# Performance work log

Measured on AMD Instinct MI355X. Metric: run time of the kernel, lower is better.

The kernel has to match this reference:

```python
import jax, jax.numpy as jnp
import numpy as np

D = 768      # embedding_dim
M = 3072     # mlp_dim
G = 4        # num_expert_groups
E = 8        # experts_per_group
KG = 2       # k_groups
KE = 4       # k_experts
EPS = 1e-6   # gate weight threshold from the torch module


def setup_inputs() -> dict:
    key = jax.random.key(0)
    ks = jax.random.split(key, 9)
    x = jax.random.normal(ks[0], (1, 1024, D), dtype=jnp.float32)
    Wg = jax.random.normal(ks[1], (D, G), dtype=jnp.float32) * 0.02
    bg = jax.random.normal(ks[2], (G,), dtype=jnp.float32) * 0.01
    We = jax.random.normal(ks[3], (G, D, E), dtype=jnp.float32) * 0.02
    be = jax.random.normal(ks[4], (G, E), dtype=jnp.float32) * 0.01
    W1 = jax.random.normal(ks[5], (G, E, D, M), dtype=jnp.float32) * 0.02
    b1 = jax.random.normal(ks[6], (G, E, M), dtype=jnp.float32) * 0.01
    W2 = jax.random.normal(ks[7], (G, E, M, D), dtype=jnp.float32) * 0.02
    b2 = jax.random.normal(ks[8], (G, E, D), dtype=jnp.float32) * 0.01
    return {"x": x, "Wg": Wg, "bg": bg, "We": We, "be": be,
            "W1": W1, "b1": b1, "W2": W2, "b2": b2}


def _topk_gates(logits, k):
    # top-k logits -> softmax over the k entries, then zero out weights < 1e-6
    top, idx = jax.lax.top_k(logits, k)
    gates = jax.nn.softmax(top, axis=-1)
    gates = jnp.where(gates >= EPS, gates, jnp.zeros_like(gates))
    return gates, idx


def reference(x, Wg, bg, We, be, W1, b1, W2, b2):
    orig_shape = x.shape
    xf = x.reshape(-1, D)  # [N, D]

    # ---- level 1: group gating (eval mode: clean logits, no noise) ----
    glog = xf @ Wg + bg                      # [N, G]
    ggates, gidx = _topk_gates(glog, KG)     # [N, KG]
    gw = jnp.einsum('nk,nkg->ng', ggates,
                    jax.nn.one_hot(gidx, G, dtype=xf.dtype))  # dense [N, G]

    # ---- level 2: expert gating within each group ----
    # computed densely for all groups; unselected groups get zero group weight
    elog = jnp.einsum('nd,gde->nge', xf, We) + be  # [N, G, E]
    egates, eidx = _topk_gates(elog, KE)            # [N, G, KE]
    ew = jnp.einsum('ngk,ngke->nge', egates,
                    jax.nn.one_hot(eidx, E, dtype=xf.dtype))  # dense [N, G, E]

    combine = gw[:, :, None] * ew  # [N, G, E] combine weights

    # ---- expert MLPs (dense compute, combine-weighted sum) ----
    y = jnp.zeros_like(xf)
    for g in range(G):  # small fixed loop over expert groups
        h = jax.nn.gelu(jnp.einsum('nd,edm->enm', xf, W1[g]) + b1[g][:, None, :],
                        approximate=False)               # [E, N, M]
        o = jnp.einsum('enm,emd->end', h, W2[g]) + b2[g][:, None, :]  # [E, N, D]
        y = y + jnp.einsum('end,ne->nd', o, combine[:, g, :])
    return y.reshape(orig_shape)
```

## Files before the change

### kernel.cpp

```cpp
#include <hip/hip_runtime.h>
#include <hip/hip_bf16.h>
#include <math.h>

#define NTOK 1024
#define DDIM 768
#define MDIM 3072
#define GN 4
#define EN 8
#define NEXP 32
#define NPAIR 8192
#define EPSW 1e-6f
#define MAXRB 96

typedef __attribute__((ext_vector_type(4))) float f32x4;
typedef __attribute__((ext_vector_type(4))) int   i32x4;
typedef __attribute__((ext_vector_type(4))) unsigned short u16x4;
typedef __attribute__((ext_vector_type(8))) __bf16 bf16x8;

__device__ __forceinline__ unsigned short f2bf(float f) {
  unsigned u = __builtin_bit_cast(unsigned, f);
  u += 0x7FFFu + ((u >> 16) & 1u);
  return (unsigned short)(u >> 16);
}

__device__ __forceinline__ unsigned cvt_pk_bf16(float lo, float hi) {
  unsigned r;
  asm volatile("v_cvt_pk_bf16_f32 %0, %1, %2" : "=v"(r) : "v"(lo), "v"(hi));
  return r;
}

__device__ __forceinline__ void gld_lds16(const void* g, void* l) {
  __builtin_amdgcn_global_load_lds(
      (const __attribute__((address_space(1))) void*)g,
      (__attribute__((address_space(3))) void*)l, 16, 0, 0);
}

__global__ void init_kernel(int* __restrict__ p) { p[threadIdx.x] = 0; }

__global__ __launch_bounds__(256) void zero_y(float* __restrict__ y) {
  ((f32x4*)y)[blockIdx.x * 256 + threadIdx.x] = (f32x4){0.f, 0.f, 0.f, 0.f};
}

__global__ __launch_bounds__(256) void x2bf(const float* __restrict__ x,
                                            unsigned short* __restrict__ xb) {
  const int i = (blockIdx.x * 256 + threadIdx.x) * 16;
#pragma unroll
  for (int j = 0; j < 4; ++j) {
    const f32x4 v = *(const f32x4*)(x + i + j * 4);
    u16x4 p = { f2bf(v.x), f2bf(v.y), f2bf(v.z), f2bf(v.w) };
    *(u16x4*)(xb + i + j * 4) = p;
  }
}

__global__ __launch_bounds__(256) void gating_kernel(
    const float* __restrict__ x, const float* __restrict__ Wg,
    const float* __restrict__ bg, const float* __restrict__ We,
    const float* __restrict__ be, int* __restrict__ counts,
    int* __restrict__ pair_e, float* __restrict__ pair_w)
{
  __shared__ float xr[DDIM];
  __shared__ float logits[36];
  const int n = blockIdx.x;
  const int tid = threadIdx.x;
  const float* xp = x + (size_t)n * DDIM;
  for (int d = tid; d < DDIM; d += 256) xr[d] = xp[d];
  __syncthreads();

  const int w = tid >> 6, lane = tid & 63;
  for (int j = 0; j < 9; ++j) {
    const int o = w + 4 * j;
    float s = 0.f;
    if (o < 4) {
      for (int d = lane; d < DDIM; d += 64) s += xr[d] * Wg[d * GN + o];
    } else {
      const int g = (o - 4) >> 3, e = (o - 4) & 7;
      const float* wp = We + (size_t)g * DDIM * EN + e;
      for (int d = lane; d < DDIM; d += 64) s += xr[d] * wp[d * EN];
    }
    for (int off = 32; off; off >>= 1) s += __shfl_xor(s, off);
    if (lane == 0) logits[o] = s + ((o < 4) ? bg[o] : be[o - 4]);
  }
  __syncthreads();

  if (tid == 0) {
    float gl[4];
    for (int i = 0; i < 4; ++i) gl[i] = logits[i];
    int i0 = 0;
    for (int i = 1; i < 4; ++i) if (gl[i] > gl[i0]) i0 = i;
    int i1 = -1;
    for (int i = 0; i < 4; ++i) {
      if (i == i0) continue;
      if (i1 < 0 || gl[i] > gl[i1]) i1 = i;
    }
    const float m = gl[i0];
    const float e1 = expf(gl[i1] - m);
    const float s2 = 1.f + e1;
    float gv[2] = { 1.f / s2, e1 / s2 };
    int gi[2] = { i0, i1 };
    for (int r = 0; r < 2; ++r) if (gv[r] < EPSW) gv[r] = 0.f;

    for (int r = 0; r < 2; ++r) {
      const int g = gi[r];
      float el[8];
      for (int e = 0; e < 8; ++e) el[e] = logits[4 + g * 8 + e];
      int sel[4];
      for (int q = 0; q < 4; ++q) {
        int best = -1;
        for (int e = 0; e < 8; ++e) {
          bool used = false;
          for (int p = 0; p < q; ++p) if (sel[p] == e) used = true;
          if (used) continue;
          if (best < 0 || el[e] > el[best]) best = e;
        }
        sel[q] = best;
      }
      const float mm = el[sel[0]];
      float ex[4]; float ss = 0.f;
      for (int q = 0; q < 4; ++q) { ex[q] = expf(el[sel[q]] - mm); ss += ex[q]; }
      for (int q = 0; q < 4; ++q) {
        float ew = ex[q] / ss;
        if (ew < EPSW) ew = 0.f;
        const int gbl = g * 8 + sel[q];
        const int j = r * 4 + q;
        pair_e[n * 8 + j] = gbl;
        pair_w[n * 8 + j] = gv[r] * ew;
        atomicAdd(&counts[gbl], 1);
      }
    }
  }
}

__global__ void scan_kernel(const int* __restrict__ counts, int* __restrict__ offsets,
                            int* __restrict__ rb_ge, int* __restrict__ rb_by,
                            int* __restrict__ nrb)
{
  if (threadIdx.x == 0) {
    int a = 0, n = 0;
    for (int e = 0; e < NEXP; ++e) {
      offsets[e] = a;
      const int c = counts[e];
      a += c;
      for (int b = 0; b * 128 < c; ++b) { rb_ge[n] = e; rb_by[n] = b; ++n; }
    }
    *nrb = n;
  }
}

__global__ __launch_bounds__(256) void scatter_kernel(
    const int* __restrict__ pair_e, const float* __restrict__ pair_w,
    const int* __restrict__ offsets, int* __restrict__ cursor,
    int* __restrict__ slot_tok, float* __restrict__ slot_w)
{
  const int idx = blockIdx.x * 256 + threadIdx.x;
  if (idx < NPAIR) {
    const int e = pair_e[idx];
    const int s = offsets[e] + atomicAdd(&cursor[e], 1);
    slot_tok[s] = idx >> 3;
    slot_w[s] = pair_w[idx];
  }
}

template<int K, int NLD, int EPI, int GATHER, int KS>
__global__ __launch_bounds__(256, 2) void moe_gemm_gl(
    const unsigned short* __restrict__ Abase, const float* __restrict__ W,
    const float* __restrict__ bias, const int* __restrict__ counts,
    const int* __restrict__ offsets, const float* __restrict__ slot_w,
    const int* __restrict__ slot_tok, const int* __restrict__ rb_ge,
    const int* __restrict__ rb_by, const int* __restrict__ nrb,
    unsigned short* __restrict__ Hout, float* __restrict__ Yout)
{
  constexpr int KC = K / KS;
  constexpr int NT = KC / 32;
  constexpr int ABY = 8192;
  constexpr int FBY = 16384;
  constexpr int BBY = 8192;
  constexpr int BUFB = ABY + FBY + BBY;

  const int rb = blockIdx.x;
  if (rb >= *nrb) return;
  const int ge = rb_ge[rb];
  const int by = rb_by[rb];
  const int cnt = counts[ge];
  const int off = offsets[ge];
  const int nb = blockIdx.y;
  const int ks = (KS > 1) ? blockIdx.z : 0;
  const int kbase = ks * KC;
  const int tid = threadIdx.x;

  __shared__ __align__(16) unsigned char lds[2 * BUFB];

  const unsigned short* asrc[2];
#pragma unroll
  for (int i = 0; i < 2; ++i) {
    const int q = tid + 256 * i;
    const int m = q >> 2, c = q & 3;
    const int sc = c ^ ((m ^ (m >> 2)) & 3);
    int gr = by * 128 + m; if (gr >= cnt) gr = cnt - 1;
    const int row = GATHER ? slot_tok[off + gr] : (off + gr);
    asrc[i] = Abase + (size_t)row * K + kbase + sc * 8;
  }

  const float* fsrc[4];
#pragma unroll
  for (int i = 0; i < 4; ++i) {
    const int q = tid + 256 * i;
    fsrc[i] = W + (size_t)ge * K * NLD + (size_t)(kbase + (q >> 5)) * NLD
                + nb * 128 + (q & 31) * 4;
  }

  const int tn = tid & 127;
  const int tk0 = (tid >> 7) * 16;
  const int tsn = (tn ^ (tn >> 2)) & 3;

  const int w = tid >> 6, lane = tid & 63;
  const int wr = (w >> 1) * 64, wc = (w & 1) * 64;
  const int l15 = lane & 15, l4 = lane >> 4;
  int aoff[4], boff[4];
#pragma unroll
  for (int mf = 0; mf < 4; ++mf) {
    const int m = wr + mf * 16 + l15;
    aoff[mf] = m * 64 + ((l4 ^ ((m ^ (m >> 2)) & 3)) * 16);
  }
#pragma unroll
  for (int nf = 0; nf < 4; ++nf) {
    const int n = wc + nf * 16 + l15;
    boff[nf] = ABY + FBY + n * 64 + ((l4 ^ ((n ^ (n >> 2)) & 3)) * 16);
  }

  f32x4 acc[4][4];
#pragma unroll
  for (int mf = 0; mf < 4; ++mf)
#pragma unroll
    for (int nf = 0; nf < 4; ++nf)
      acc[mf][nf] = (f32x4){0.f, 0.f, 0.f, 0.f};

#define ISSUE(T, BASE) { \
    _Pragma("unroll") \
    for (int i = 0; i < 2; ++i) \
      gld_lds16(asrc[i] + (size_t)(T) * 32, (BASE) + (tid + 256 * i) * 16); \
    _Pragma("unroll") \
    for (int i = 0; i < 4; ++i) \
      gld_lds16(fsrc[i] + (size_t)(T) * 32 * NLD, (BASE) + ABY + (tid + 256 * i) * 16); }
#define TRANS(BASE) { \
    const float* fp = (const float*)((BASE) + ABY); \
    unsigned char* bb = (BASE) + ABY + FBY; \
    float fv[16]; \
    _Pragma("unroll") \
    for (int j = 0; j < 16; ++j) fv[j] = fp[(tk0 + j) * 128 + tn]; \
    _Pragma("unroll") \
    for (int jp = 0; jp < 8; ++jp) { \
      const unsigned wv = cvt_pk_bf16(fv[2 * jp], fv[2 * jp + 1]); \
      const int c = (tk0 * 2 + 4 * jp) >> 4; \
      *(unsigned*)(bb + tn * 64 + ((c ^ tsn) * 16) + ((4 * jp) & 15)) = wv; } }
#define COMPUTE(BASE) { bf16x8 afr[4], bfr[4]; _Pragma("unroll") \
    for (int mf = 0; mf < 4; ++mf) \
      afr[mf] = __builtin_bit_cast(bf16x8, *(const i32x4*)((BASE) + aoff[mf])); \
    _Pragma("unroll") \
    for (int nf = 0; nf < 4; ++nf) \
      bfr[nf] = __builtin_bit_cast(bf16x8, *(const i32x4*)((BASE) + boff[nf])); \
    _Pragma("unroll") \
    for (int mf = 0; mf < 4; ++mf) { _Pragma("unroll") \
      for (int nf = 0; nf < 4; ++nf) \
        acc[mf][nf] = __builtin_amdgcn_mfma_f32_16x16x32_bf16( \
            afr[mf], bfr[nf], acc[mf][nf], 0, 0, 0); } }

  ISSUE(0, lds);

  for (int t = 0; t < NT; ++t) {
    unsigned char* buf = lds + (t & 1) * BUFB;
    unsigned char* obuf = lds + ((t + 1) & 1) * BUFB;
    asm volatile("s_waitcnt vmcnt(0)" ::: "memory");
    __builtin_amdgcn_s_barrier();
    asm volatile("" ::: "memory");
    if (t + 1 < NT) ISSUE(t + 1, obuf);
    TRANS(buf);
    asm volatile("s_waitcnt lgkmcnt(0)" ::: "memory");
    __builtin_amdgcn_s_barrier();
    asm volatile("" ::: "memory");
    COMPUTE(buf);
  }
#undef ISSUE
#undef TRANS
#undef COMPUTE

#pragma unroll
  for (int mf = 0; mf < 4; ++mf) {
    const int rb2 = by * 128 + wr + mf * 16 + l4 * 4;
    if constexpr (EPI == 0) {
#pragma unroll
      for (int nf = 0; nf < 4; ++nf) {
        const int col = nb * 128 + wc + nf * 16 + l15;
        const float bv = bias[(size_t)ge * NLD + col];
#pragma unroll
        for (int j = 0; j < 4; ++j) {
          const int r = rb2 + j;
          if (r < cnt) {
            const float v = acc[mf][nf][j] + bv;
            const float gl = 0.5f * v * (1.f + erff(v * 0.70710678118654752f));
            Hout[(size_t)(off + r) * NLD + col] = f2bf(gl);
          }
        }
      }
    } else {
#pragma unroll
      for (int j = 0; j < 4; ++j) {
        const int r = rb2 + j;
        if (r < cnt) {
          const int slot = off + r;
          const float sw = slot_w[slot];
          const int tok = slot_tok[slot];
#pragma unroll
          for (int nf = 0; nf < 4; ++nf) {
            const int col = nb * 128 + wc + nf * 16 + l15;
            const float bv = (ks == 0) ? bias[(size_t)ge * NLD + col] : 0.f;
            atomicAdd(&Yout[(size_t)tok * DDIM + col], sw * (acc[mf][nf][j] + bv));
          }
        }
      }
    }
  }
}

extern "C" void kernel_launch(void* const* d_in, const int* in_sizes, int n_in,
                              void* d_out, int out_size, void* d_ws, size_t ws_size,
                              hipStream_t stream)
{
  const float* x  = (const float*)d_in[0];
  const float* Wg = (const float*)d_in[1];
  const float* bg = (const float*)d_in[2];
  const float* We = (const float*)d_in[3];
  const float* be = (const float*)d_in[4];
  const float* W1 = (const float*)d_in[5];
  const float* b1 = (const float*)d_in[6];
  const float* W2 = (const float*)d_in[7];
  const float* b2 = (const float*)d_in[8];
  float* y = (float*)d_out;

  char* ws = (char*)d_ws;
  int*   counts   = (int*)(ws + 0);
  int*   offsets  = (int*)(ws + 128);
  int*   cursor   = (int*)(ws + 256);
  int*   nrb      = (int*)(ws + 384);
  int*   rb_ge    = (int*)(ws + 512);
  int*   rb_by    = (int*)(ws + 896);
  int*   pair_e   = (int*)(ws + 2048);
  float* pair_w   = (float*)(ws + 34816);
  int*   slot_tok = (int*)(ws + 67584);
  float* slot_w   = (float*)(ws + 100352);
  unsigned short* xb = (unsigned short*)(ws + 135168);
  unsigned short* H  = (unsigned short*)(ws + 12715008);

  init_kernel<<<1, 256, 0, stream>>>((int*)ws);
  zero_y<<<NTOK * DDIM / 1024, 256, 0, stream>>>(y);
  x2bf<<<NTOK * DDIM / 4096, 256, 0, stream>>>(x, xb);
  gating_kernel<<<NTOK, 256, 0, stream>>>(x, Wg, bg, We, be, counts, pair_e, pair_w);
  scan_kernel<<<1, 64, 0, stream>>>(counts, offsets, rb_ge, rb_by, nrb);
  scatter_kernel<<<NPAIR / 256, 256, 0, stream>>>(pair_e, pair_w, offsets, cursor,
                                                  slot_tok, slot_w);

  moe_gemm_gl<DDIM, MDIM, 0, 1, 1><<<dim3(MAXRB, MDIM / 128, 1), 256, 0, stream>>>(
      xb, W1, b1, counts, offsets, nullptr, slot_tok, rb_ge, rb_by, nrb, H, nullptr);
  moe_gemm_gl<MDIM, DDIM, 1, 0, 2><<<dim3(MAXRB, DDIM / 128, 2), 256, 0, stream>>>(
      H, W2, b2, counts, offsets, slot_w, slot_tok, rb_ge, rb_by, nrb, nullptr, y);
}
```

Baseline: 562.1 us.

## Pre-repack expert weights to transposed bf16 and deepen GEMM prefetch pipeline

Adds a repack kernel that transposes each expert's fp32 W1/W2 into a K-contiguous bf16 buffer before each GEMM. The grouped GEMM then loads bf16 B tiles straight into LDS, with no per-tile fp32-to-bf16 transpose in LDS. The main loop now keeps two tiles in flight (prefetch distance 2) with a partial vmcnt wait. The cost is a full pass over all 32 experts' weights every call, including experts that get no tokens, plus extra workspace.

```diff
diff --git a/kernel.cpp b/kernel.cpp
--- a/kernel.cpp
+++ b/kernel.cpp
@@ -23,16 +23,15 @@
   return (unsigned short)(u >> 16);
 }
 
-__device__ __forceinline__ unsigned cvt_pk_bf16(float lo, float hi) {
-  unsigned r;
-  asm volatile("v_cvt_pk_bf16_f32 %0, %1, %2" : "=v"(r) : "v"(lo), "v"(hi));
-  return r;
-}
-
 __device__ __forceinline__ void gld_lds16(const void* g, void* l) {
   __builtin_amdgcn_global_load_lds(
       (const __attribute__((address_space(1))) void*)g,
       (__attribute__((address_space(3))) void*)l, 16, 0, 0);
+}
+
+template<int N>
+__device__ __forceinline__ void wait_vmcnt() {
+  asm volatile("s_waitcnt vmcnt(%0)" :: "n"(N) : "memory");
 }
 
 __global__ void init_kernel(int* __restrict__ p) { p[threadIdx.x] = 0; }
@@ -160,9 +159,36 @@
   }
 }
 
+template<int R, int C>
+__global__ __launch_bounds__(256) void repack_kernel(
+    const float* __restrict__ W, unsigned short* __restrict__ Wt)
+{
+  __shared__ float tile[32][33];
+  const int ge = blockIdx.z;
+  const int rt = blockIdx.y, ct = blockIdx.x;
+  const int tid = threadIdx.x;
+  {
+    const int r = tid >> 3, c4 = tid & 7;
+    const f32x4 v = *(const f32x4*)(W + (size_t)ge * R * C
+                                      + (size_t)(rt * 32 + r) * C + ct * 32 + c4 * 4);
+#pragma unroll
+    for (int j = 0; j < 4; ++j) tile[r][c4 * 4 + j] = v[j];
+  }
+  __syncthreads();
+  {
+    const int n = tid >> 3, k4 = tid & 7;
+    u16x4 p;
+    p.x = f2bf(tile[k4 * 4 + 0][n]);
+    p.y = f2bf(tile[k4 * 4 + 1][n]);
+    p.z = f2bf(tile[k4 * 4 + 2][n]);
+    p.w = f2bf(tile[k4 * 4 + 3][n]);
+    *(u16x4*)(Wt + (size_t)ge * R * C + (size_t)(ct * 32 + n) * R + rt * 32 + k4 * 4) = p;
+  }
+}
+
 template<int K, int NLD, int EPI, int GATHER, int KS>
-__global__ __launch_bounds__(256, 2) void moe_gemm_gl(
-    const unsigned short* __restrict__ Abase, const float* __restrict__ W,
+__global__ __launch_bounds__(256) void moe_gemm_bt2(
+    const unsigned short* __restrict__ A, const unsigned short* __restrict__ Bt,
     const float* __restrict__ bias, const int* __restrict__ counts,
     const int* __restrict__ offsets, const float* __restrict__ slot_w,
     const int* __restrict__ slot_tok, const int* __restrict__ rb_ge,
@@ -172,9 +198,7 @@
   constexpr int KC = K / KS;
   constexpr int NT = KC / 32;
   constexpr int ABY = 8192;
-  constexpr int FBY = 16384;
-  constexpr int BBY = 8192;
-  constexpr int BUFB = ABY + FBY + BBY;
+  constexpr int BUFB = 16384;
 
   const int rb = blockIdx.x;
   if (rb >= *nrb) return;
@@ -190,6 +214,7 @@
   __shared__ __align__(16) unsigned char lds[2 * BUFB];
 
   const unsigned short* asrc[2];
+  const unsigned short* bsrc[2];
 #pragma unroll
   for (int i = 0; i < 2; ++i) {
     const int q = tid + 256 * i;
@@ -197,20 +222,9 @@
     const int sc = c ^ ((m ^ (m >> 2)) & 3);
     int gr = by * 128 + m; if (gr >= cnt) gr = cnt - 1;
     const int row = GATHER ? slot_tok[off + gr] : (off + gr);
-    asrc[i] = Abase + (size_t)row * K + kbase + sc * 8;
-  }
-
-  const float* fsrc[4];
-#pragma unroll
-  for (int i = 0; i < 4; ++i) {
-    const int q = tid + 256 * i;
-    fsrc[i] = W + (size_t)ge * K * NLD + (size_t)(kbase + (q >> 5)) * NLD
-                + nb * 128 + (q & 31) * 4;
-  }
-
-  const int tn = tid & 127;
-  const int tk0 = (tid >> 7) * 16;
-  const int tsn = (tn ^ (tn >> 2)) & 3;
+    asrc[i] = A + (size_t)row * K + kbase + sc * 8;
+    bsrc[i] = Bt + (size_t)ge * NLD * K + (size_t)(nb * 128 + m) * K + kbase + sc * 8;
+  }
 
   const int w = tid >> 6, lane = tid & 63;
   const int wr = (w >> 1) * 64, wc = (w & 1) * 64;
@@ -224,7 +238,7 @@
 #pragma unroll
   for (int nf = 0; nf < 4; ++nf) {
     const int n = wc + nf * 16 + l15;
-    boff[nf] = ABY + FBY + n * 64 + ((l4 ^ ((n ^ (n >> 2)) & 3)) * 16);
+    boff[nf] = ABY + n * 64 + ((l4 ^ ((n ^ (n >> 2)) & 3)) * 16);
   }
 
   f32x4 acc[4][4];
@@ -234,24 +248,10 @@
     for (int nf = 0; nf < 4; ++nf)
       acc[mf][nf] = (f32x4){0.f, 0.f, 0.f, 0.f};
 
-#define ISSUE(T, BASE) { \
-    _Pragma("unroll") \
-    for (int i = 0; i < 2; ++i) \
-      gld_lds16(asrc[i] + (size_t)(T) * 32, (BASE) + (tid + 256 * i) * 16); \
-    _Pragma("unroll") \
-    for (int i = 0; i < 4; ++i) \
-      gld_lds16(fsrc[i] + (size_t)(T) * 32 * NLD, (BASE) + ABY + (tid + 256 * i) * 16); }
-#define TRANS(BASE) { \
-    const float* fp = (const float*)((BASE) + ABY); \
-    unsigned char* bb = (BASE) + ABY + FBY; \
-    float fv[16]; \
-    _Pragma("unroll") \
-    for (int j = 0; j < 16; ++j) fv[j] = fp[(tk0 + j) * 128 + tn]; \
-    _Pragma("unroll") \
-    for (int jp = 0; jp < 8; ++jp) { \
-      const unsigned wv = cvt_pk_bf16(fv[2 * jp], fv[2 * jp + 1]); \
-      const int c = (tk0 * 2 + 4 * jp) >> 4; \
-      *(unsigned*)(bb + tn * 64 + ((c ^ tsn) * 16) + ((4 * jp) & 15)) = wv; } }
+#define ISSUE(T, B) { _Pragma("unroll") \
+    for (int i = 0; i < 2; ++i) { \
+      gld_lds16(asrc[i] + (size_t)(T) * 32, lds + (B) * BUFB + (tid + 256 * i) * 16); \
+      gld_lds16(bsrc[i] + (size_t)(T) * 32, lds + (B) * BUFB + ABY + (tid + 256 * i) * 16); } }
 #define COMPUTE(BASE) { bf16x8 afr[4], bfr[4]; _Pragma("unroll") \
     for (int mf = 0; mf < 4; ++mf) \
       afr[mf] = __builtin_bit_cast(bf16x8, *(const i32x4*)((BASE) + aoff[mf])); \
@@ -264,23 +264,19 @@
         acc[mf][nf] = __builtin_amdgcn_mfma_f32_16x16x32_bf16( \
             afr[mf], bfr[nf], acc[mf][nf], 0, 0, 0); } }
 
-  ISSUE(0, lds);
+  ISSUE(0, 0);
+  ISSUE(1, 1);
 
   for (int t = 0; t < NT; ++t) {
-    unsigned char* buf = lds + (t & 1) * BUFB;
-    unsigned char* obuf = lds + ((t + 1) & 1) * BUFB;
-    asm volatile("s_waitcnt vmcnt(0)" ::: "memory");
+    if (t + 1 < NT) wait_vmcnt<4>(); else wait_vmcnt<0>();
     __builtin_amdgcn_s_barrier();
     asm volatile("" ::: "memory");
-    if (t + 1 < NT) ISSUE(t + 1, obuf);
-    TRANS(buf);
-    asm volatile("s_waitcnt lgkmcnt(0)" ::: "memory");
+    COMPUTE(lds + (t & 1) * BUFB);
+    asm volatile("" ::: "memory");
     __builtin_amdgcn_s_barrier();
-    asm volatile("" ::: "memory");
-    COMPUTE(buf);
+    if (t + 2 < NT) ISSUE(t + 2, t & 1);
   }
 #undef ISSUE
-#undef TRANS
 #undef COMPUTE
 
 #pragma unroll
@@ -349,6 +345,7 @@
   float* slot_w   = (float*)(ws + 100352);
   unsigned short* xb = (unsigned short*)(ws + 135168);
   unsigned short* H  = (unsigned short*)(ws + 12715008);
+  unsigned short* Wt = (unsigned short*)(ws + 63046656);
 
   init_kernel<<<1, 256, 0, stream>>>((int*)ws);
   zero_y<<<NTOK * DDIM / 1024, 256, 0, stream>>>(y);
@@ -358,8 +355,10 @@
   scatter_kernel<<<NPAIR / 256, 256, 0, stream>>>(pair_e, pair_w, offsets, cursor,
                                                   slot_tok, slot_w);
 
-  moe_gemm_gl<DDIM, MDIM, 0, 1, 1><<<dim3(MAXRB, MDIM / 128, 1), 256, 0, stream>>>(
-      xb, W1, b1, counts, offsets, nullptr, slot_tok, rb_ge, rb_by, nrb, H, nullptr);
-  moe_gemm_gl<MDIM, DDIM, 1, 0, 2><<<dim3(MAXRB, DDIM / 128, 2), 256, 0, stream>>>(
-      H, W2, b2, counts, offsets, slot_w, slot_tok, rb_ge, rb_by, nrb, nullptr, y);
-}
+  repack_kernel<DDIM, MDIM><<<dim3(MDIM / 32, DDIM / 32, NEXP), 256, 0, stream>>>(W1, Wt);
+  moe_gemm_bt2<DDIM, MDIM, 0, 1, 1><<<dim3(MAXRB, MDIM / 128, 1), 256, 0, stream>>>(
+      xb, Wt, b1, counts, offsets, nullptr, slot_tok, rb_ge, rb_by, nrb, H, nullptr);
+  repack_kernel<MDIM, DDIM><<<dim3(DDIM / 32, MDIM / 32, NEXP), 256, 0, stream>>>(W2, Wt);
+  moe_gemm_bt2<MDIM, DDIM, 1, 0, 2><<<dim3(MAXRB, DDIM / 128, 2), 256, 0, stream>>>(
+      H, Wt, b2, counts, offsets, slot_w, slot_tok, rb_ge, rb_by, nrb, nullptr, y);
+}
```

Result: slower. 585.1 us (+4.1%).
